# Kernel tuning notes

Measured on AMD Instinct MI355X. Metric: run time of the kernel, lower is better.

The kernel has to match this reference:

```python
import math
import jax, jax.numpy as jnp
import numpy as np

B, T, C, H = 2, 2048, 1024, 16

def setup_inputs() -> dict:
    key = jax.random.key(0)
    k1, k2, k3 = jax.random.split(key, 3)
    x = jax.random.normal(k1, (B, T, C), dtype=jnp.float32)
    W_kqv = jax.random.normal(k2, (C, 3 * C), dtype=jnp.float32) * (1.0 / math.sqrt(C))
    W_proj = jax.random.normal(k3, (C, C), dtype=jnp.float32) * (1.0 / math.sqrt(C))
    b_proj = jnp.zeros((C,), dtype=jnp.float32)
    return {"x": x, "W_kqv": W_kqv, "W_proj": W_proj, "b_proj": b_proj}

def reference(x, W_kqv, W_proj, b_proj):
    Bx, Tx, Cx = x.shape
    hs = Cx // H  # head size
    q, k, v = jnp.split(x @ W_kqv, 3, axis=2)  # each (B,T,C)
    # (B,T,C) -> (B,H,T,hs)
    q = q.reshape(Bx, Tx, H, hs).transpose(0, 2, 1, 3)
    k = k.reshape(Bx, Tx, H, hs).transpose(0, 2, 1, 3)
    v = v.reshape(Bx, Tx, H, hs).transpose(0, 2, 1, 3)
    attn = jnp.einsum('bhqd,bhkd->bhqk', q, k) / math.sqrt(hs)  # (B,H,T,T)
    causal = jnp.tril(jnp.ones((Tx, Tx), dtype=bool))
    attn = jnp.where(causal, attn, -jnp.inf)
    attn = jax.nn.softmax(attn, axis=-1)
    y = jnp.einsum('bhqk,bhkd->bhqd', attn, v)  # (B,H,T,hs)
    y = y.transpose(0, 2, 1, 3).reshape(Bx, Tx, Cx)
    return y @ W_proj + b_proj
```

## Files before the change

kernel.cpp:

```cpp
#include <hip/hip_runtime.h>


typedef unsigned short u16;
typedef unsigned int u32;
typedef __bf16 bf16x8 __attribute__((ext_vector_type(8)));
typedef float f32x4 __attribute__((ext_vector_type(4)));
typedef u32 u32x4 __attribute__((ext_vector_type(4)));
typedef u32 u32x2 __attribute__((ext_vector_type(2)));
typedef u16 u16x4 __attribute__((ext_vector_type(4)));

__device__ __forceinline__ u16 f2bf(float f) {
  u32 u = __float_as_uint(f);
  u32 r = u + 0x7FFFu + ((u >> 16) & 1u);
  return (u16)(r >> 16);
}

__device__ __forceinline__ u32 cvt_pk_bf16(float a, float b) {
  u32 r;
  asm("v_cvt_pk_bf16_f32 %0, %1, %2" : "=v"(r) : "v"(a), "v"(b));
  return r;
}

__device__ __forceinline__ bf16x8 ld_bf8(const u16* p) {
  union { u32x4 u; bf16x8 b; } x;
  x.u = *(const u32x4*)p;
  return x.b;
}

__device__ __forceinline__ void gld_lds16(const u16* g, u16* l) {
  __builtin_amdgcn_global_load_lds(
      (const __attribute__((address_space(1))) u32*)g,
      (__attribute__((address_space(3))) u32*)l, 16, 0, 0);
}

__device__ __forceinline__ void convT_body(const float* __restrict__ src,
                                           u16* __restrict__ dst, int R, int Cc,
                                           int r0, int c0, float* ls ) {
  int t = threadIdx.x;
  for (int u = t; u < 1024; u += 256) {
    int r = u >> 4, cs = (u & 15) << 2;
    float4 v = *(const float4*)&src[(size_t)(r0 + r) * Cc + (c0 + cs)];
    ls[r * 65 + cs] = v.x; ls[r * 65 + cs + 1] = v.y;
    ls[r * 65 + cs + 2] = v.z; ls[r * 65 + cs + 3] = v.w;
  }
  __syncthreads();
  for (int u = t; u < 1024; u += 256) {
    int n = u >> 4, ks = (u & 15) << 2;
    u16x4 o;
    o.x = f2bf(ls[ks * 65 + n]); o.y = f2bf(ls[(ks + 1) * 65 + n]);
    o.z = f2bf(ls[(ks + 2) * 65 + n]); o.w = f2bf(ls[(ks + 3) * 65 + n]);
    *(u16x4*)&dst[(size_t)(c0 + n) * R + (r0 + ks)] = o;
  }
}

__global__ __launch_bounds__(256) void prep_kernel(
    const float* __restrict__ x, const float* __restrict__ Wkqv,
    const float* __restrict__ Wproj, u16* __restrict__ xb,
    u16* __restrict__ wkqvT, u16* __restrict__ wprojT) {
  __shared__ float ls[64 * 65];
  int bx = blockIdx.x;
  if (bx < 2048) {
    int idx = bx * 256 + threadIdx.x;
    const float4* s4 = (const float4*)x;
    float4 a = s4[2 * idx], b = s4[2 * idx + 1];
    union { u16 h[8]; u32x4 v; } pk;
    pk.h[0] = f2bf(a.x); pk.h[1] = f2bf(a.y); pk.h[2] = f2bf(a.z); pk.h[3] = f2bf(a.w);
    pk.h[4] = f2bf(b.x); pk.h[5] = f2bf(b.y); pk.h[6] = f2bf(b.z); pk.h[7] = f2bf(b.w);
    *(u32x4*)&xb[(size_t)idx * 8] = pk.v;
  } else if (bx < 2816) {
    int idx = bx - 2048;
    convT_body(Wkqv, wkqvT, 1024, 3072, (idx & 15) * 64, (idx >> 4) * 64, ls);
  } else {
    int idx = bx - 2816;
    convT_body(Wproj, wprojT, 1024, 1024, (idx & 15) * 64, (idx >> 4) * 64, ls);
  }
}

__global__ __launch_bounds__(256) void qkv_gemm_kernel(
    const u16* __restrict__ A, const u16* __restrict__ Bt,
    u16* __restrict__ Qh, u16* __restrict__ Kh, u16* __restrict__ Vh, float qscale) {
  constexpr int K = 1024;
  __shared__ __align__(16) u16 As[128 * 32];
  __shared__ __align__(16) u16 Bs[128 * 32];
  int t = threadIdx.x;
  int wave = t >> 6, lane = t & 63, quad = lane >> 4, l16 = lane & 15;
  int wm = (wave >> 1) << 6, wn = (wave & 1) << 6;
  int m0 = blockIdx.x * 128, n0 = blockIdx.y * 128;
  f32x4 acc[4][4] = {};
  int u0 = t, u1 = t + 256;
  int ra0 = u0 >> 2, ca0 = ((u0 & 3) ^ ((u0 >> 3) & 3)) << 3;
  int ra1 = u1 >> 2, ca1 = ((u1 & 3) ^ ((u1 >> 3) & 3)) << 3;
  int swq = (quad ^ ((l16 >> 1) & 3)) << 3;
  for (int k0 = 0; k0 < K; k0 += 32) {
    gld_lds16(&A[(size_t)(m0 + ra0) * K + k0 + ca0], &As[u0 * 8]);
    gld_lds16(&A[(size_t)(m0 + ra1) * K + k0 + ca1], &As[u1 * 8]);
    gld_lds16(&Bt[(size_t)(n0 + ra0) * K + k0 + ca0], &Bs[u0 * 8]);
    gld_lds16(&Bt[(size_t)(n0 + ra1) * K + k0 + ca1], &Bs[u1 * 8]);
    __syncthreads();
    bf16x8 af[4], bfr[4];
    for (int r = 0; r < 4; ++r) af[r] = ld_bf8(&As[(wm + r * 16 + l16) * 32 + swq]);
    for (int c = 0; c < 4; ++c) bfr[c] = ld_bf8(&Bs[(wn + c * 16 + l16) * 32 + swq]);
    for (int r = 0; r < 4; ++r)
      for (int c = 0; c < 4; ++c)
        acc[r][c] = __builtin_amdgcn_mfma_f32_16x16x32_bf16(af[r], bfr[c], acc[r][c], 0, 0, 0);
    __syncthreads();
  }
  for (int r = 0; r < 4; ++r) {
    int rowbase = m0 + wm + r * 16 + quad * 4;
    for (int c = 0; c < 4; ++c) {
      int col = n0 + wn + c * 16 + l16;
      int seg = col >> 10;
      int cc = col & 1023;
      int h = cc >> 6, d = cc & 63;
      for (int i = 0; i < 4; ++i) {
        int row = rowbase + i;
        int b = row >> 11, tt = row & 2047;
        size_t off = (((size_t)(b * 16 + h)) * 2048 + tt) * 64 + d;
        float v = acc[r][c][i];
        if (seg == 0)      Qh[off] = f2bf(v * qscale);
        else if (seg == 1) Kh[off] = f2bf(v);
        else               Vh[off] = f2bf(v);
      }
    }
  }
}

__global__ __launch_bounds__(256) void vT_kernel(const u16* __restrict__ Vh,
                                                 u16* __restrict__ Vt) {
  __shared__ __align__(16) u16 ls[64 * 72];
  int t = threadIdx.x;
  int t0 = blockIdx.x * 64, bh = blockIdx.y;
  const u16* in = Vh + ((size_t)bh * 2048 + t0) * 64;
  for (int u = t; u < 512; u += 256) {
    int row = u >> 3, col = (u & 7) << 3;
    *(u32x4*)&ls[row * 72 + col] = *(const u32x4*)&in[(size_t)row * 64 + col];
  }
  __syncthreads();
  for (int u = t; u < 512; u += 256) {
    int d = u >> 3, tc = (u & 7) << 3;
    union { u16 h[8]; u32x4 v; } pk;
    for (int j = 0; j < 8; ++j) pk.h[j] = ls[(tc + j) * 72 + d];
    *(u32x4*)&Vt[((size_t)bh * 64 + d) * 2048 + t0 + tc] = pk.v;
  }
}

__global__ __launch_bounds__(256) void proj_gemm_kernel(
    const u16* __restrict__ A, const u16* __restrict__ Bt,
    float* __restrict__ out, const float* __restrict__ bias) {
  constexpr int K = 1024;
  __shared__ __align__(16) u16 As[64 * 32];
  __shared__ __align__(16) u16 Bs[64 * 32];
  int t = threadIdx.x;
  int wave = t >> 6, lane = t & 63, quad = lane >> 4, l16 = lane & 15;
  int wm = (wave >> 1) << 5, wn = (wave & 1) << 5;
  int m0 = blockIdx.x * 64, n0 = blockIdx.y * 64;
  f32x4 acc[2][2] = {};
  int u0 = t;
  int ra0 = u0 >> 2, ca0 = ((u0 & 3) ^ ((u0 >> 3) & 3)) << 3;
  int swq = (quad ^ ((l16 >> 1) & 3)) << 3;
  for (int k0 = 0; k0 < K; k0 += 32) {
    gld_lds16(&A[(size_t)(m0 + ra0) * K + k0 + ca0], &As[u0 * 8]);
    gld_lds16(&Bt[(size_t)(n0 + ra0) * K + k0 + ca0], &Bs[u0 * 8]);
    __syncthreads();
    bf16x8 af[2], bfr[2];
    for (int r = 0; r < 2; ++r) af[r] = ld_bf8(&As[(wm + r * 16 + l16) * 32 + swq]);
    for (int c = 0; c < 2; ++c) bfr[c] = ld_bf8(&Bs[(wn + c * 16 + l16) * 32 + swq]);
    for (int r = 0; r < 2; ++r)
      for (int c = 0; c < 2; ++c)
        acc[r][c] = __builtin_amdgcn_mfma_f32_16x16x32_bf16(af[r], bfr[c], acc[r][c], 0, 0, 0);
    __syncthreads();
  }
  for (int r = 0; r < 2; ++r) {
    int rowbase = m0 + wm + r * 16 + quad * 4;
    for (int c = 0; c < 2; ++c) {
      int col = n0 + wn + c * 16 + l16;
      float bv = bias[col];
      for (int i = 0; i < 4; ++i)
        out[(size_t)(rowbase + i) * 1024 + col] = acc[r][c][i] + bv;
    }
  }
}

__global__ __launch_bounds__(256, 4) void flash_kernel(
    const u16* __restrict__ Qh, const u16* __restrict__ Kh, const u16* __restrict__ Vt,
    u16* __restrict__ yb, float* __restrict__ Opart) {
  __shared__ __align__(16) u16 Ks[64 * 64];
  __shared__ __align__(16) u16 Vs[64 * 64];
  int t = threadIdx.x, wave = t >> 6, lane = t & 63, quad = lane >> 4, l16 = lane & 15;
  const unsigned char JT[22] = {9, 8, 7, 47, 63, 46, 62, 6, 45, 61, 44, 60,
                                5, 43, 59, 42, 58, 4, 3, 2, 1, 0};
  int id = blockIdx.x;
  int g = id / 176, r = id % 176;
  int bh = g * 8 + (r & 7);
  int jx = r >> 3;
  int code = JT[jx];
  int qtile = code & 15;
  int half = (code >> 4) & 1;
  bool partial = (code >> 5) != 0;
  int nkv = 2 * qtile + 2, mid = qtile + 1;
  int kvs = (partial && half) ? mid : 0;
  int kve = partial ? (half ? nkv : mid) : nkv;
  int sidx = 15 - qtile;
  int q0 = qtile << 7;
  const u16* Qb = Qh + (size_t)bh * 2048 * 64;
  const u16* Kb = Kh + (size_t)bh * 2048 * 64;
  const u16* Vb = Vt + (size_t)bh * 64 * 2048;
  int qlo = q0 + wave * 32;
  int qhi = qlo + 31;
  bf16x8 qa0, qa1, qa2, qa3;
  {
    int qr0 = qlo + l16;
    qa0 = ld_bf8(&Qb[(size_t)qr0 * 64 + quad * 8]);
    qa1 = ld_bf8(&Qb[(size_t)qr0 * 64 + 32 + quad * 8]);
    int qr1 = qr0 + 16;
    qa2 = ld_bf8(&Qb[(size_t)qr1 * 64 + quad * 8]);
    qa3 = ld_bf8(&Qb[(size_t)qr1 * 64 + 32 + quad * 8]);
  }
  f32x4 oacc0[4] = {}, oacc1[4] = {};
  float lsum0 = 0.f, lsum1 = 0.f;
  int u0 = wave * 128 + lane, u1 = u0 + 64;
  int r0 = u0 >> 3, p0 = u0 & 7, cb0 = (p0 - r0) & 7;
  int r1s = u1 >> 3, p1 = u1 & 7, cb1 = (p1 - r1s) & 7;
  int vsub = (quad & 1) * 4;
  int vc0 = quad >> 1;
  for (int j = kvs; j < kve; ++j) {
    int kv0 = j << 6;
    __syncthreads();
    gld_lds16(&Kb[(size_t)(kv0 + r0) * 64 + cb0 * 8], &Ks[u0 * 8]);
    gld_lds16(&Kb[(size_t)(kv0 + r1s) * 64 + cb1 * 8], &Ks[u1 * 8]);
    gld_lds16(&Vb[(size_t)r0 * 2048 + kv0 + cb0 * 8], &Vs[u0 * 8]);
    gld_lds16(&Vb[(size_t)r1s * 2048 + kv0 + cb1 * 8], &Vs[u1 * 8]);
    __syncthreads();
    if (kv0 > qhi) continue;
    bool maskit = (kv0 + 63 > qlo);
    u32 w0[4][2], w1[4][2];
    for (int c = 0; c < 4; ++c) {
      int krow = c * 16 + l16;
      bf16x8 kb0 = ld_bf8(&Ks[krow * 64 + ((quad + krow) & 7) * 8]);
      bf16x8 kb1 = ld_bf8(&Ks[krow * 64 + ((quad + 4 + krow) & 7) * 8]);
      f32x4 z0 = {0.f, 0.f, 0.f, 0.f}, z1 = {0.f, 0.f, 0.f, 0.f};
      z0 = __builtin_amdgcn_mfma_f32_16x16x32_bf16(kb0, qa0, z0, 0, 0, 0);
      z0 = __builtin_amdgcn_mfma_f32_16x16x32_bf16(kb1, qa1, z0, 0, 0, 0);
      z1 = __builtin_amdgcn_mfma_f32_16x16x32_bf16(kb0, qa2, z1, 0, 0, 0);
      z1 = __builtin_amdgcn_mfma_f32_16x16x32_bf16(kb1, qa3, z1, 0, 0, 0);
      float pe0[4], pe1[4];
      if (maskit) {
        int qg0 = qlo + l16, qg1 = qg0 + 16;
        for (int i = 0; i < 4; ++i) {
          int kv = kv0 + c * 16 + quad * 4 + i;
          float a = __builtin_amdgcn_exp2f(z0[i]);
          float b = __builtin_amdgcn_exp2f(z1[i]);
          if (kv > qg0) a = 0.f;
          if (kv > qg1) b = 0.f;
          lsum0 += a; lsum1 += b;
          pe0[i] = a; pe1[i] = b;
        }
      } else {
        for (int i = 0; i < 4; ++i) {
          float a = __builtin_amdgcn_exp2f(z0[i]);
          float b = __builtin_amdgcn_exp2f(z1[i]);
          lsum0 += a; lsum1 += b;
          pe0[i] = a; pe1[i] = b;
        }
      }
      w0[c][0] = cvt_pk_bf16(pe0[0], pe0[1]); w0[c][1] = cvt_pk_bf16(pe0[2], pe0[3]);
      w1[c][0] = cvt_pk_bf16(pe1[0], pe1[1]); w1[c][1] = cvt_pk_bf16(pe1[2], pe1[3]);
    }
    union { u32 uu[4]; bf16x8 b; } pf00, pf01, pf10, pf11;
    pf00.uu[0] = w0[0][0]; pf00.uu[1] = w0[0][1]; pf00.uu[2] = w0[1][0]; pf00.uu[3] = w0[1][1];
    pf01.uu[0] = w0[2][0]; pf01.uu[1] = w0[2][1]; pf01.uu[2] = w0[3][0]; pf01.uu[3] = w0[3][1];
    pf10.uu[0] = w1[0][0]; pf10.uu[1] = w1[0][1]; pf10.uu[2] = w1[1][0]; pf10.uu[3] = w1[1][1];
    pf11.uu[0] = w1[2][0]; pf11.uu[1] = w1[2][1]; pf11.uu[2] = w1[3][0]; pf11.uu[3] = w1[3][1];
    for (int dt = 0; dt < 4; ++dt) {
      int vrow = dt * 16 + l16;
      int rbase = vrow * 64 + vsub;
      union { u32x2 lo2; struct { u32 a, b; }; } h0lo, h0hi, h1lo, h1hi;
      h0lo.lo2 = *(const u32x2*)&Vs[rbase + (((vc0)     + vrow) & 7) * 8];
      h0hi.lo2 = *(const u32x2*)&Vs[rbase + (((vc0 + 2) + vrow) & 7) * 8];
      h1lo.lo2 = *(const u32x2*)&Vs[rbase + (((vc0 + 4) + vrow) & 7) * 8];
      h1hi.lo2 = *(const u32x2*)&Vs[rbase + (((vc0 + 6) + vrow) & 7) * 8];
      union { u32 uu[4]; bf16x8 b; } va0, va1;
      va0.uu[0] = h0lo.a; va0.uu[1] = h0lo.b; va0.uu[2] = h0hi.a; va0.uu[3] = h0hi.b;
      va1.uu[0] = h1lo.a; va1.uu[1] = h1lo.b; va1.uu[2] = h1hi.a; va1.uu[3] = h1hi.b;
      oacc0[dt] = __builtin_amdgcn_mfma_f32_16x16x32_bf16(va0.b, pf00.b, oacc0[dt], 0, 0, 0);
      oacc0[dt] = __builtin_amdgcn_mfma_f32_16x16x32_bf16(va1.b, pf01.b, oacc0[dt], 0, 0, 0);
      oacc1[dt] = __builtin_amdgcn_mfma_f32_16x16x32_bf16(va0.b, pf10.b, oacc1[dt], 0, 0, 0);
      oacc1[dt] = __builtin_amdgcn_mfma_f32_16x16x32_bf16(va1.b, pf11.b, oacc1[dt], 0, 0, 0);
    }
  }
  lsum0 += __shfl_xor(lsum0, 16);
  lsum0 += __shfl_xor(lsum0, 32);
  lsum1 += __shfl_xor(lsum1, 16);
  lsum1 += __shfl_xor(lsum1, 32);
  if (partial) {
    float* Op = Opart + ((size_t)(bh * 6 + sidx) * 2 + half) * 8320;
    int ql = wave * 32 + l16;
    for (int dt = 0; dt < 4; ++dt)
      *(f32x4*)&Op[ql * 64 + dt * 16 + quad * 4] = oacc0[dt];
    for (int dt = 0; dt < 4; ++dt)
      *(f32x4*)&Op[(ql + 16) * 64 + dt * 16 + quad * 4] = oacc1[dt];
    if (quad == 0) { Op[8192 + ql] = lsum0; Op[8192 + ql + 16] = lsum1; }
  } else {
    int b = bh >> 4, hd = bh & 15;
    float inv0 = 1.0f / lsum0, inv1 = 1.0f / lsum1;
    int qq0 = qlo + l16;
    size_t ro0 = ((size_t)(b * 2048 + qq0)) * 1024 + hd * 64;
    size_t ro1 = ro0 + (size_t)16 * 1024;
    for (int dt = 0; dt < 4; ++dt) {
      u32x2 pr;
      pr.x = cvt_pk_bf16(oacc0[dt][0] * inv0, oacc0[dt][1] * inv0);
      pr.y = cvt_pk_bf16(oacc0[dt][2] * inv0, oacc0[dt][3] * inv0);
      *(u32x2*)&yb[ro0 + dt * 16 + quad * 4] = pr;
      pr.x = cvt_pk_bf16(oacc1[dt][0] * inv1, oacc1[dt][1] * inv1);
      pr.y = cvt_pk_bf16(oacc1[dt][2] * inv1, oacc1[dt][3] * inv1);
      *(u32x2*)&yb[ro1 + dt * 16 + quad * 4] = pr;
    }
  }
}

__global__ __launch_bounds__(256) void combine_kernel(const float* __restrict__ Opart,
                                                      u16* __restrict__ yb) {
  int sidx = blockIdx.x, bh = blockIdx.y, t = threadIdx.x;
  int qtile = 15 - sidx;
  const float* A = Opart + (size_t)(bh * 6 + sidx) * 2 * 8320;
  const float* Bp = A + 8320;
  int q = t >> 1, d0 = (t & 1) << 5;
  float inv = 1.0f / (A[8192 + q] + Bp[8192 + q]);
  int b = bh >> 4, h = bh & 15;
  size_t off = ((size_t)(b * 2048 + (qtile << 7) + q)) * 1024 + h * 64 + d0;
  union { u16 hh[32]; u32x4 v[4]; } pk;
  for (int k = 0; k < 32; ++k)
    pk.hh[k] = f2bf((A[q * 64 + d0 + k] + Bp[q * 64 + d0 + k]) * inv);
  for (int s = 0; s < 4; ++s)
    *(u32x4*)&yb[off + s * 8] = pk.v[s];
}

extern "C" void kernel_launch(void* const* d_in, const int* in_sizes, int n_in,
                              void* d_out, int out_size, void* d_ws, size_t ws_size,
                              hipStream_t stream) {
  const float* x     = (const float*)d_in[0];
  const float* Wkqv  = (const float*)d_in[1];
  const float* Wproj = (const float*)d_in[2];
  const float* bproj = (const float*)d_in[3];
  float* out = (float*)d_out;

  u16* ws     = (u16*)d_ws;
  u16* xb     = ws;
  u16* wkqvT  = xb + (size_t)4096 * 1024;
  u16* wprojT = wkqvT + (size_t)3072 * 1024;
  u16* Qh     = wprojT + (size_t)1024 * 1024;
  u16* Kh     = Qh + (size_t)32 * 2048 * 64;
  u16* Vt     = Kh + (size_t)32 * 2048 * 64;
  u16* yb     = Vt + (size_t)32 * 2048 * 64;
  u16* Vh     = yb;
  float* Opart = (float*)ws;

  const float QSCALE = 0.18033688011112042f;

  prep_kernel<<<3072, 256, 0, stream>>>(x, Wkqv, Wproj, xb, wkqvT, wprojT);
  qkv_gemm_kernel<<<dim3(32, 24), 256, 0, stream>>>(xb, wkqvT, Qh, Kh, Vh, QSCALE);
  vT_kernel<<<dim3(32, 32), 256, 0, stream>>>(Vh, Vt);
  flash_kernel<<<704, 256, 0, stream>>>(Qh, Kh, Vt, yb, Opart);
  combine_kernel<<<dim3(6, 32), 256, 0, stream>>>(Opart, yb);
  proj_gemm_kernel<<<dim3(64, 16), 256, 0, stream>>>(yb, wprojT, out, bproj);
}
```

Before: 181.4 us.

## Double-buffer K/V tiles in flash kernel to overlap loads with compute

Doubles the LDS K and V tiles and issues the global-to-LDS loads for the next KV block before computing on the current one, using one barrier per iteration instead of two. The aim is to hide global memory latency behind the MFMA and exp work. LDS use doubles to 32 KB per block, which may reduce occupancy under the 4-blocks-per-CU launch bound.

```diff
diff --git a/kernel.cpp b/kernel.cpp
--- a/kernel.cpp
+++ b/kernel.cpp
@@ -184,8 +184,8 @@
 __global__ __launch_bounds__(256, 4) void flash_kernel(
     const u16* __restrict__ Qh, const u16* __restrict__ Kh, const u16* __restrict__ Vt,
     u16* __restrict__ yb, float* __restrict__ Opart) {
-  __shared__ __align__(16) u16 Ks[64 * 64];
-  __shared__ __align__(16) u16 Vs[64 * 64];
+  __shared__ __align__(16) u16 Ks[2][64 * 64];
+  __shared__ __align__(16) u16 Vs[2][64 * 64];
   int t = threadIdx.x, wave = t >> 6, lane = t & 63, quad = lane >> 4, l16 = lane & 15;
   const unsigned char JT[22] = {9, 8, 7, 47, 63, 46, 62, 6, 45, 61, 44, 60,
                                 5, 43, 59, 42, 58, 4, 3, 2, 1, 0};
@@ -223,21 +223,36 @@
   int r1s = u1 >> 3, p1 = u1 & 7, cb1 = (p1 - r1s) & 7;
   int vsub = (quad & 1) * 4;
   int vc0 = quad >> 1;
+  {
+    int kv0 = kvs << 6;
+    gld_lds16(&Kb[(size_t)(kv0 + r0) * 64 + cb0 * 8], &Ks[0][u0 * 8]);
+    gld_lds16(&Kb[(size_t)(kv0 + r1s) * 64 + cb1 * 8], &Ks[0][u1 * 8]);
+    gld_lds16(&Vb[(size_t)r0 * 2048 + kv0 + cb0 * 8], &Vs[0][u0 * 8]);
+    gld_lds16(&Vb[(size_t)r1s * 2048 + kv0 + cb1 * 8], &Vs[0][u1 * 8]);
+  }
   for (int j = kvs; j < kve; ++j) {
+    int p = (j - kvs) & 1;
+    asm volatile("s_waitcnt vmcnt(0)" ::: "memory");
+    __builtin_amdgcn_s_barrier();
+    asm volatile("" ::: "memory");
+    if (j + 1 < kve) {
+      int kn0 = (j + 1) << 6;
+      int pn = p ^ 1;
+      gld_lds16(&Kb[(size_t)(kn0 + r0) * 64 + cb0 * 8], &Ks[pn][u0 * 8]);
+      gld_lds16(&Kb[(size_t)(kn0 + r1s) * 64 + cb1 * 8], &Ks[pn][u1 * 8]);
+      gld_lds16(&Vb[(size_t)r0 * 2048 + kn0 + cb0 * 8], &Vs[pn][u0 * 8]);
+      gld_lds16(&Vb[(size_t)r1s * 2048 + kn0 + cb1 * 8], &Vs[pn][u1 * 8]);
+    }
     int kv0 = j << 6;
-    __syncthreads();
-    gld_lds16(&Kb[(size_t)(kv0 + r0) * 64 + cb0 * 8], &Ks[u0 * 8]);
-    gld_lds16(&Kb[(size_t)(kv0 + r1s) * 64 + cb1 * 8], &Ks[u1 * 8]);
-    gld_lds16(&Vb[(size_t)r0 * 2048 + kv0 + cb0 * 8], &Vs[u0 * 8]);
-    gld_lds16(&Vb[(size_t)r1s * 2048 + kv0 + cb1 * 8], &Vs[u1 * 8]);
-    __syncthreads();
     if (kv0 > qhi) continue;
+    const u16* Ksp = Ks[p];
+    const u16* Vsp = Vs[p];
     bool maskit = (kv0 + 63 > qlo);
     u32 w0[4][2], w1[4][2];
     for (int c = 0; c < 4; ++c) {
       int krow = c * 16 + l16;
-      bf16x8 kb0 = ld_bf8(&Ks[krow * 64 + ((quad + krow) & 7) * 8]);
-      bf16x8 kb1 = ld_bf8(&Ks[krow * 64 + ((quad + 4 + krow) & 7) * 8]);
+      bf16x8 kb0 = ld_bf8(&Ksp[krow * 64 + ((quad + krow) & 7) * 8]);
+      bf16x8 kb1 = ld_bf8(&Ksp[krow * 64 + ((quad + 4 + krow) & 7) * 8]);
       f32x4 z0 = {0.f, 0.f, 0.f, 0.f}, z1 = {0.f, 0.f, 0.f, 0.f};
       z0 = __builtin_amdgcn_mfma_f32_16x16x32_bf16(kb0, qa0, z0, 0, 0, 0);
       z0 = __builtin_amdgcn_mfma_f32_16x16x32_bf16(kb1, qa1, z0, 0, 0, 0);
@@ -275,10 +290,10 @@
       int vrow = dt * 16 + l16;
       int rbase = vrow * 64 + vsub;
       union { u32x2 lo2; struct { u32 a, b; }; } h0lo, h0hi, h1lo, h1hi;
-      h0lo.lo2 = *(const u32x2*)&Vs[rbase + (((vc0)     + vrow) & 7) * 8];
-      h0hi.lo2 = *(const u32x2*)&Vs[rbase + (((vc0 + 2) + vrow) & 7) * 8];
-      h1lo.lo2 = *(const u32x2*)&Vs[rbase + (((vc0 + 4) + vrow) & 7) * 8];
-      h1hi.lo2 = *(const u32x2*)&Vs[rbase + (((vc0 + 6) + vrow) & 7) * 8];
+      h0lo.lo2 = *(const u32x2*)&Vsp[rbase + (((vc0)     + vrow) & 7) * 8];
+      h0hi.lo2 = *(const u32x2*)&Vsp[rbase + (((vc0 + 2) + vrow) & 7) * 8];
+      h1lo.lo2 = *(const u32x2*)&Vsp[rbase + (((vc0 + 4) + vrow) & 7) * 8];
+      h1hi.lo2 = *(const u32x2*)&Vsp[rbase + (((vc0 + 6) + vrow) & 7) * 8];
       union { u32 uu[4]; bf16x8 b; } va0, va1;
       va0.uu[0] = h0lo.a; va0.uu[1] = h0lo.b; va0.uu[2] = h0hi.a; va0.uu[3] = h0hi.b;
       va1.uu[0] = h1lo.a; va1.uu[1] = h1lo.b; va1.uu[2] = h1hi.a; va1.uu[3] = h1hi.b;
```

After: 181.1 us. No clear change (-0.2%).

## Load K/V fragments directly from global memory instead of staging through LDS

Applied to the files above, without the earlier changes.

Removes the shared-memory K/V tiles and the two block-wide barriers per KV step; each wave now reads its K and V MFMA fragments straight from global memory (relying on L1/L2 for reuse across the 4 waves). Each wave also trims its loop bound to the last KV tile it needs under the causal mask, so waves no longer spin through tiles they skip. The launch-bounds occupancy hint is dropped. This trades LDS traffic and synchronisation for redundant global/cache loads (4 waves each read the same tiles) and less coalesced 8-byte V reads.

```diff
diff --git a/kernel.cpp b/kernel.cpp
--- a/kernel.cpp
+++ b/kernel.cpp
@@ -181,11 +181,9 @@
   }
 }
 
-__global__ __launch_bounds__(256, 4) void flash_kernel(
+__global__ __launch_bounds__(256) void flash_kernel(
     const u16* __restrict__ Qh, const u16* __restrict__ Kh, const u16* __restrict__ Vt,
     u16* __restrict__ yb, float* __restrict__ Opart) {
-  __shared__ __align__(16) u16 Ks[64 * 64];
-  __shared__ __align__(16) u16 Vs[64 * 64];
   int t = threadIdx.x, wave = t >> 6, lane = t & 63, quad = lane >> 4, l16 = lane & 15;
   const unsigned char JT[22] = {9, 8, 7, 47, 63, 46, 62, 6, 45, 61, 44, 60,
                                 5, 43, 59, 42, 58, 4, 3, 2, 1, 0};
@@ -218,26 +216,17 @@
   }
   f32x4 oacc0[4] = {}, oacc1[4] = {};
   float lsum0 = 0.f, lsum1 = 0.f;
-  int u0 = wave * 128 + lane, u1 = u0 + 64;
-  int r0 = u0 >> 3, p0 = u0 & 7, cb0 = (p0 - r0) & 7;
-  int r1s = u1 >> 3, p1 = u1 & 7, cb1 = (p1 - r1s) & 7;
   int vsub = (quad & 1) * 4;
   int vc0 = quad >> 1;
-  for (int j = kvs; j < kve; ++j) {
+  int kveW = kve < ((qhi >> 6) + 1) ? kve : ((qhi >> 6) + 1);
+  for (int j = kvs; j < kveW; ++j) {
     int kv0 = j << 6;
-    __syncthreads();
-    gld_lds16(&Kb[(size_t)(kv0 + r0) * 64 + cb0 * 8], &Ks[u0 * 8]);
-    gld_lds16(&Kb[(size_t)(kv0 + r1s) * 64 + cb1 * 8], &Ks[u1 * 8]);
-    gld_lds16(&Vb[(size_t)r0 * 2048 + kv0 + cb0 * 8], &Vs[u0 * 8]);
-    gld_lds16(&Vb[(size_t)r1s * 2048 + kv0 + cb1 * 8], &Vs[u1 * 8]);
-    __syncthreads();
-    if (kv0 > qhi) continue;
     bool maskit = (kv0 + 63 > qlo);
     u32 w0[4][2], w1[4][2];
     for (int c = 0; c < 4; ++c) {
-      int krow = c * 16 + l16;
-      bf16x8 kb0 = ld_bf8(&Ks[krow * 64 + ((quad + krow) & 7) * 8]);
-      bf16x8 kb1 = ld_bf8(&Ks[krow * 64 + ((quad + 4 + krow) & 7) * 8]);
+      int krow = kv0 + c * 16 + l16;
+      bf16x8 kb0 = ld_bf8(&Kb[(size_t)krow * 64 + quad * 8]);
+      bf16x8 kb1 = ld_bf8(&Kb[(size_t)krow * 64 + 32 + quad * 8]);
       f32x4 z0 = {0.f, 0.f, 0.f, 0.f}, z1 = {0.f, 0.f, 0.f, 0.f};
       z0 = __builtin_amdgcn_mfma_f32_16x16x32_bf16(kb0, qa0, z0, 0, 0, 0);
       z0 = __builtin_amdgcn_mfma_f32_16x16x32_bf16(kb1, qa1, z0, 0, 0, 0);
@@ -273,12 +262,12 @@
     pf11.uu[0] = w1[2][0]; pf11.uu[1] = w1[2][1]; pf11.uu[2] = w1[3][0]; pf11.uu[3] = w1[3][1];
     for (int dt = 0; dt < 4; ++dt) {
       int vrow = dt * 16 + l16;
-      int rbase = vrow * 64 + vsub;
+      const u16* vb = &Vb[(size_t)vrow * 2048 + kv0 + vc0 * 8 + vsub];
       union { u32x2 lo2; struct { u32 a, b; }; } h0lo, h0hi, h1lo, h1hi;
-      h0lo.lo2 = *(const u32x2*)&Vs[rbase + (((vc0)     + vrow) & 7) * 8];
-      h0hi.lo2 = *(const u32x2*)&Vs[rbase + (((vc0 + 2) + vrow) & 7) * 8];
-      h1lo.lo2 = *(const u32x2*)&Vs[rbase + (((vc0 + 4) + vrow) & 7) * 8];
-      h1hi.lo2 = *(const u32x2*)&Vs[rbase + (((vc0 + 6) + vrow) & 7) * 8];
+      h0lo.lo2 = *(const u32x2*)&vb[0];
+      h0hi.lo2 = *(const u32x2*)&vb[16];
+      h1lo.lo2 = *(const u32x2*)&vb[32];
+      h1hi.lo2 = *(const u32x2*)&vb[48];
       union { u32 uu[4]; bf16x8 b; } va0, va1;
       va0.uu[0] = h0lo.a; va0.uu[1] = h0lo.b; va0.uu[2] = h0hi.a; va0.uu[3] = h0hi.b;
       va1.uu[0] = h1lo.a; va1.uu[1] = h1lo.b; va1.uu[2] = h1hi.a; va1.uu[3] = h1hi.b;
```

After: 268.9 us. 48.2% more time.
